# Kernel tuning notes

Hardware: AMD Instinct MI355X
Metric: run time of the kernel (lower is better)

The kernel has to match this reference:

```python
import jax, jax.numpy as jnp
import numpy as np

BS, QLEN, DIM, NH = 4, 2048, 1024, 16
DH = DIM // NH
NEG = float(np.finfo(np.float32).min)


def setup_inputs() -> dict:
    key = jax.random.key(0)
    ks = jax.random.split(key, 10)
    s = 1.0 / np.sqrt(DIM)
    return {
        "hidden_states": jax.random.normal(ks[0], (BS, QLEN, DIM), jnp.float32),
        "attention_mask": jnp.ones((BS, QLEN), jnp.int32),
        "Wq": jax.random.normal(ks[1], (DIM, DIM), jnp.float32) * s,
        "bq": jnp.zeros((DIM,), jnp.float32),
        "Wk": jax.random.normal(ks[2], (DIM, DIM), jnp.float32) * s,
        "bk": jnp.zeros((DIM,), jnp.float32),
        "Wv": jax.random.normal(ks[3], (DIM, DIM), jnp.float32) * s,
        "bv": jnp.zeros((DIM,), jnp.float32),
        "Wo": jax.random.normal(ks[4], (DIM, DIM), jnp.float32) * s,
        "bo": jnp.zeros((DIM,), jnp.float32),
    }


def _heads(x, bs):
    # [bs, len, dim] -> [bs, n_heads, len, dim_per_head]
    return x.reshape(bs, -1, NH, DH).transpose(0, 2, 1, 3)


def reference(hidden_states, attention_mask, Wq, bq, Wk, bk, Wv, bv, Wo, bo):
    bs, qlen, dim = hidden_states.shape
    q = _heads(hidden_states @ Wq.T + bq, bs) / jnp.sqrt(jnp.asarray(DH, hidden_states.dtype))
    k = _heads(hidden_states @ Wk.T + bk, bs)
    v = _heads(hidden_states @ Wv.T + bv, bs)
    scores = jnp.einsum("bhqd,bhkd->bhqk", q, k)  # [bs, nh, qlen, klen]
    mask = (attention_mask == 0)[:, None, None, :]  # [bs,1,1,klen]
    scores = jnp.where(mask, NEG, scores)
    weights = jax.nn.softmax(scores.astype(jnp.float32), axis=-1).astype(scores.dtype)
    context = jnp.einsum("bhqk,bhkd->bhqd", weights, v)
    context = context.transpose(0, 2, 1, 3).reshape(bs, qlen, dim)
    return context @ Wo.T + bo
```

## Files before the change

kernel.cpp:

```cpp
#include <hip/hip_runtime.h>
#include <hip/hip_bf16.h>

#define BS 4
#define QLEN 2048
#define DIM 1024
#define NH 16
#define DH 64

typedef __attribute__((ext_vector_type(8))) short bf16x8;
typedef __attribute__((ext_vector_type(4))) float f32x4;
typedef __attribute__((ext_vector_type(16))) float f32x16;
typedef __attribute__((ext_vector_type(2))) unsigned int u32x2;
typedef __attribute__((ext_vector_type(4))) unsigned int u32x4;
typedef unsigned short u16;
typedef unsigned int u32;
typedef unsigned long long u64;

#define LOG2E 1.44269504088896f

__device__ __forceinline__ u32 cvtpk_bf16(float lo, float hi) {
    u32 r;
    asm("v_cvt_pk_bf16_f32 %0, %1, %2" : "=v"(r) : "v"(lo), "v"(hi));
    return r;
}
__device__ __forceinline__ u16 f2bf_hw(float f) { return (u16)cvtpk_bf16(f, f); }

__device__ __forceinline__ void async_lds16(const void* gp, void* lp) {
    __builtin_amdgcn_global_load_lds(
        (const __attribute__((address_space(1))) u32*)(u64)gp,
        (__attribute__((address_space(3))) u32*)(u32)(u64)lp,
        16, 0, 0);
}

__global__ void cvt_fused(const float* __restrict__ H,
                          const float* __restrict__ W0, const float* __restrict__ W1,
                          const float* __restrict__ W2, const float* __restrict__ W3,
                          u16* __restrict__ Hb,
                          u16* __restrict__ D0, u16* __restrict__ D1,
                          u16* __restrict__ D2, u16* __restrict__ D3) {
    const int h4 = (BS * QLEN * DIM) / 4;
    int i = blockIdx.x * blockDim.x + threadIdx.x;
    const float* s;
    u16* d;
    int off;
    if (i < h4) { s = H; d = Hb; off = i; }
    else {
        int j = i - h4;
        int ws = j >> 18;
        off = j & 262143;
        s = ws == 0 ? W0 : ws == 1 ? W1 : ws == 2 ? W2 : W3;
        d = ws == 0 ? D0 : ws == 1 ? D1 : ws == 2 ? D2 : D3;
    }
    float4 v = ((const float4*)s)[off];
    uint2 o;
    o.x = cvtpk_bf16(v.x, v.y);
    o.y = cvtpk_bf16(v.z, v.w);
    ((uint2*)d)[off] = o;
}

__global__ void mask_prep(const int* __restrict__ mask, float* __restrict__ maskF,
                          int* __restrict__ flags) {
    const int tile = blockIdx.x;
    const int lane = threadIdx.x;
    const int idx = tile * 64 + lane;
    const int v = mask[idx];
    maskF[idx] = v ? 1.0f : 0.0f;
    u64 bal = __ballot(v == 0);
    if (lane == 0) flags[tile] = (bal != 0ull) ? 1 : 0;
}

__global__ __launch_bounds__(256) void gemm_qkv(
    const u16* __restrict__ Hb,
    const u16* __restrict__ Wq, const u16* __restrict__ Wk, const u16* __restrict__ Wv,
    const float* __restrict__ bq, const float* __restrict__ bk, const float* __restrict__ bvv,
    u16* __restrict__ Qb, u16* __restrict__ KF, u16* __restrict__ VF)
{
    __shared__ __align__(16) u16 As[2][128 * 32];
    __shared__ __align__(16) u16 Bs[2][128 * 32];
    const int z = blockIdx.z;
    const u16* W = z == 0 ? Wq : z == 1 ? Wk : Wv;
    const float* bias = z == 0 ? bq : z == 1 ? bk : bvv;
    const int t = threadIdx.x;
    const int w = t >> 6, lane = t & 63;
    const int lr = lane & 15, lg = lane >> 4;
    const int m0 = blockIdx.y * 128, n0 = blockIdx.x * 128;
    const int wm = (w >> 1) * 64, wn = (w & 1) * 64;
    const int srow = w * 16 + (lane >> 2);
    const int sk = (lane & 3) * 8;

    f32x4 acc[4][4] = {};

    auto STAGE = [&](int B, int kt) {
        async_lds16(Hb + (u64)(m0 + srow) * DIM + kt + sk,      &As[B][(w * 16) * 32]);
        async_lds16(Hb + (u64)(m0 + 64 + srow) * DIM + kt + sk, &As[B][(64 + w * 16) * 32]);
        async_lds16(W + (u64)(n0 + srow) * DIM + kt + sk,       &Bs[B][(w * 16) * 32]);
        async_lds16(W + (u64)(n0 + 64 + srow) * DIM + kt + sk,  &Bs[B][(64 + w * 16) * 32]);
    };

    STAGE(0, 0);
    int buf = 0;
    for (int kt = 0; kt < DIM; kt += 32) {
        asm volatile("s_waitcnt vmcnt(0)" ::: "memory");
        __builtin_amdgcn_s_barrier();
        __builtin_amdgcn_sched_barrier(0);
        if (kt + 32 < DIM) STAGE(buf ^ 1, kt + 32);
        bf16x8 a[4], b[4];
#pragma unroll
        for (int i = 0; i < 4; ++i) a[i] = *(const bf16x8*)&As[buf][(wm + i * 16 + lr) * 32 + lg * 8];
#pragma unroll
        for (int i = 0; i < 4; ++i) b[i] = *(const bf16x8*)&Bs[buf][(wn + i * 16 + lr) * 32 + lg * 8];
#pragma unroll
        for (int mi = 0; mi < 4; ++mi)
#pragma unroll
            for (int ni = 0; ni < 4; ++ni)
                acc[mi][ni] = __builtin_amdgcn_mfma_f32_16x16x32_bf16(a[mi], b[ni], acc[mi][ni], 0, 0, 0);
        buf ^= 1;
    }

#pragma unroll
    for (int mi = 0; mi < 4; ++mi)
#pragma unroll
        for (int ni = 0; ni < 4; ++ni) {
            const int col = n0 + wn + ni * 16 + lr;
            const float bb = bias[col];
#pragma unroll
            for (int r = 0; r < 4; ++r) {
                const int row = m0 + wm + mi * 16 + lg * 4 + r;
                const float v = acc[mi][ni][r] + bb;
                const int bh = (row >> 11) * NH + (col >> 6);
                const int q = row & (QLEN - 1);
                const int d = col & (DH - 1);
                if (z == 0) {
                    Qb[((u64)bh * QLEN + q) * DH + d] = f2bf_hw(v * (0.125f * LOG2E));
                } else if (z == 1) {
                    const int ktile = q >> 6, kb2 = (q >> 5) & 1, kl5 = q & 31;
                    const int c = d >> 3, dcc = c >> 1, chi = c & 1, j = d & 7;
                    KF[(u64)bh * QLEN * DH +
                       ((((u64)ktile * 2 + kb2) * 4 + dcc) * 64 + chi * 32 + kl5) * 8 + j] = f2bf_hw(v);
                } else {
                    const int ktile = q >> 6, kin = q & 63;
                    const int c = kin >> 3, kcc = c >> 1, chi = c & 1, j = kin & 7;
                    const int db = d >> 5, vl5 = d & 31;
                    VF[(u64)bh * QLEN * DH +
                       ((((u64)ktile * 2 + db) * 4 + kcc) * 64 + chi * 32 + vl5) * 8 + j] = f2bf_hw(v);
                }
            }
        }
}

__global__ __launch_bounds__(256) void gemm_o(
    const u16* __restrict__ A, const u16* __restrict__ W,
    const float* __restrict__ bias, float* __restrict__ ofp)
{
    __shared__ __align__(16) u16 As[2][128 * 32];
    __shared__ __align__(16) u16 Bs[2][128 * 32];
    const int t = threadIdx.x;
    const int w = t >> 6, lane = t & 63;
    const int lr = lane & 15, lg = lane >> 4;
    const int m0 = blockIdx.y * 128, n0 = blockIdx.x * 128;
    const int wm = (w >> 1) * 64, wn = (w & 1) * 64;
    const int srow = w * 16 + (lane >> 2);
    const int sk = (lane & 3) * 8;

    f32x4 acc[4][4] = {};

    auto STAGE = [&](int B, int kt) {
        async_lds16(A + (u64)(m0 + srow) * DIM + kt + sk,      &As[B][(w * 16) * 32]);
        async_lds16(A + (u64)(m0 + 64 + srow) * DIM + kt + sk, &As[B][(64 + w * 16) * 32]);
        async_lds16(W + (u64)(n0 + srow) * DIM + kt + sk,      &Bs[B][(w * 16) * 32]);
        async_lds16(W + (u64)(n0 + 64 + srow) * DIM + kt + sk, &Bs[B][(64 + w * 16) * 32]);
    };

    STAGE(0, 0);
    int buf = 0;
    for (int kt = 0; kt < DIM; kt += 32) {
        asm volatile("s_waitcnt vmcnt(0)" ::: "memory");
        __builtin_amdgcn_s_barrier();
        __builtin_amdgcn_sched_barrier(0);
        if (kt + 32 < DIM) STAGE(buf ^ 1, kt + 32);
        bf16x8 a[4], b[4];
#pragma unroll
        for (int i = 0; i < 4; ++i) a[i] = *(const bf16x8*)&As[buf][(wm + i * 16 + lr) * 32 + lg * 8];
#pragma unroll
        for (int i = 0; i < 4; ++i) b[i] = *(const bf16x8*)&Bs[buf][(wn + i * 16 + lr) * 32 + lg * 8];
#pragma unroll
        for (int mi = 0; mi < 4; ++mi)
#pragma unroll
            for (int ni = 0; ni < 4; ++ni)
                acc[mi][ni] = __builtin_amdgcn_mfma_f32_16x16x32_bf16(a[mi], b[ni], acc[mi][ni], 0, 0, 0);
        buf ^= 1;
    }

#pragma unroll
    for (int mi = 0; mi < 4; ++mi)
#pragma unroll
        for (int ni = 0; ni < 4; ++ni) {
            const int col = n0 + wn + ni * 16 + lr;
            const float bb = bias[col];
#pragma unroll
            for (int r = 0; r < 4; ++r) {
                const int row = m0 + wm + mi * 16 + lg * 4 + r;
                ofp[(u64)row * DIM + col] = acc[mi][ni][r] + bb;
            }
        }
}

struct KTile { bf16x8 f[2][4]; };

__global__ __launch_bounds__(256) void attn_kernel(
    const u16* __restrict__ Qb, const u16* __restrict__ KF, const u16* __restrict__ VF,
    const float* __restrict__ maskF, const int* __restrict__ mflags, u16* __restrict__ ctx)
{
    const int t = threadIdx.x;
    const int w = t >> 6, lane = t & 63;
    const int l5 = lane & 31, hi = lane >> 5;

    const int id = blockIdx.x + 16 * blockIdx.y;
    const int v = (id & 7) * 128 + (id >> 3);
    const int qt = v & 15, bh = v >> 4;
    const int b = bh >> 4, hh = bh & 15;
    const int q0 = qt * 128;

    const u16* kfl = KF + (u64)bh * QLEN * DH + (u64)lane * 8;
    const u16* vfl = VF + (u64)bh * QLEN * DH + (u64)lane * 8;
    const float* mFb = maskF + b * QLEN;
    const int* flb = mflags + b * (QLEN / 64);
    const u64 fmask = __ballot(flb[lane & 31] != 0);

    const u16* qp = Qb + ((u64)bh * QLEN + q0 + w * 32 + l5) * DH + hi * 8;
    bf16x8 bq[4];
#pragma unroll
    for (int dc = 0; dc < 4; ++dc) bq[dc] = *(const bf16x8*)(qp + dc * 16);

    f32x16 o[2] = {};
    float mrun = -3.0e38f, lsum = 0.f;

    auto loadK = [&](KTile& kk, int KT) {
        const u16* base = kfl + (u64)KT * 4096;
#pragma unroll
        for (int kb = 0; kb < 2; ++kb)
#pragma unroll
            for (int dc = 0; dc < 4; ++dc)
                kk.f[kb][dc] = *(const bf16x8*)(base + (kb * 4 + dc) * 512);
    };

    auto tile = [&](const KTile& kk, int kt64) {
        const u16* vb = vfl + (u64)kt64 * 4096;
        bf16x8 av0[4], av1[4];
#pragma unroll
        for (int kc = 0; kc < 4; ++kc) {
            av0[kc] = *(const bf16x8*)(vb + kc * 512);
            av1[kc] = *(const bf16x8*)(vb + (4 + kc) * 512);
        }

        f32x16 s0 = {}, s1 = {};
        __builtin_amdgcn_s_setprio(1);
#pragma unroll
        for (int dc = 0; dc < 4; ++dc) {
            s0 = __builtin_amdgcn_mfma_f32_32x32x16_bf16(kk.f[0][dc], bq[dc], s0, 0, 0, 0);
            s1 = __builtin_amdgcn_mfma_f32_32x32x16_bf16(kk.f[1][dc], bq[dc], s1, 0, 0, 0);
        }
        __builtin_amdgcn_s_setprio(0);

        float mx[16];
#pragma unroll
        for (int i = 0; i < 16; ++i) mx[i] = fmaxf(s0[i], s1[i]);
#pragma unroll
        for (int st = 8; st > 0; st >>= 1)
#pragma unroll
            for (int i = 0; i < 16; ++i) if (i < st) mx[i] = fmaxf(mx[i], mx[i + st]);
        const float tma = fmaxf(mx[0], __shfl_xor(mx[0], 32));

        if (!__all(tma <= mrun + 11.5415603f)) {
            const float nm = fmaxf(mrun, tma);
            const float corr = exp2f(mrun - nm);
            mrun = nm;
            lsum *= corr;
#pragma unroll
            for (int i = 0; i < 16; ++i) { o[0][i] *= corr; o[1][i] *= corr; }
        }

#pragma unroll
        for (int i = 0; i < 16; ++i) {
            s0[i] = exp2f(s0[i] - mrun);
            s1[i] = exp2f(s1[i] - mrun);
        }

        if ((fmask >> kt64) & 1ull) {
#pragma unroll
            for (int kb = 0; kb < 2; ++kb) {
                f32x16& sk = kb == 0 ? s0 : s1;
#pragma unroll
                for (int m = 0; m < 4; ++m) {
                    float4 mm = *(const float4*)&mFb[kt64 * 64 + kb * 32 + m * 8 + hi * 4];
                    sk[4 * m + 0] *= mm.x;
                    sk[4 * m + 1] *= mm.y;
                    sk[4 * m + 2] *= mm.z;
                    sk[4 * m + 3] *= mm.w;
                }
            }
        }

        {
            float ps[16];
#pragma unroll
            for (int i = 0; i < 16; ++i) ps[i] = s0[i] + s1[i];
#pragma unroll
            for (int st = 8; st > 0; st >>= 1)
#pragma unroll
                for (int i = 0; i < 16; ++i) if (i < st) ps[i] += ps[i + st];
            lsum += ps[0];
        }

        __builtin_amdgcn_s_setprio(1);
#pragma unroll
        for (int kc = 0; kc < 4; ++kc) {
            const f32x16& sk = (kc >> 1) == 0 ? s0 : s1;
            const int base = 8 * (kc & 1);
            const u32 P00 = cvtpk_bf16(sk[base + 0], sk[base + 1]);
            const u32 P01 = cvtpk_bf16(sk[base + 2], sk[base + 3]);
            const u32 P10 = cvtpk_bf16(sk[base + 4], sk[base + 5]);
            const u32 P11 = cvtpk_bf16(sk[base + 6], sk[base + 7]);
            u32x2 w02 = __builtin_amdgcn_permlane32_swap(P00, P10, false, false);
            u32x2 w13 = __builtin_amdgcn_permlane32_swap(P01, P11, false, false);
            u32x4 words;
            words.x = w02[0]; words.y = w13[0]; words.z = w02[1]; words.w = w13[1];
            const bf16x8 bp = __builtin_bit_cast(bf16x8, words);

            o[0] = __builtin_amdgcn_mfma_f32_32x32x16_bf16(av0[kc], bp, o[0], 0, 0, 0);
            o[1] = __builtin_amdgcn_mfma_f32_32x32x16_bf16(av1[kc], bp, o[1], 0, 0, 0);
        }
        __builtin_amdgcn_s_setprio(0);
    };

    KTile kA, kB;
    loadK(kA, 0);
    for (int tt = 0; tt < 32; tt += 2) {
        loadK(kB, tt + 1);
        tile(kA, tt);
        if (tt + 2 < 32) loadK(kA, tt + 2);
        tile(kB, tt + 1);
    }

    const float lall = lsum + __shfl_xor(lsum, 32);
    const float inv = 1.0f / fmaxf(lall, 1e-37f);

    u16* cp = ctx + (((u64)b * QLEN + (q0 + w * 32 + l5)) * NH + hh) * DH;
#pragma unroll
    for (int db = 0; db < 2; ++db)
#pragma unroll
        for (int m = 0; m < 4; ++m) {
            const int d0 = db * 32 + m * 8 + hi * 4;
            const u32 wA = cvtpk_bf16(o[db][4 * m + 0] * inv, o[db][4 * m + 1] * inv);
            const u32 wB = cvtpk_bf16(o[db][4 * m + 2] * inv, o[db][4 * m + 3] * inv);
            *(u32*)(cp + d0) = wA;
            *(u32*)(cp + d0 + 2) = wB;
        }
}

extern "C" void kernel_launch(void* const* d_in, const int* in_sizes, int n_in,
                              void* d_out, int out_size, void* d_ws, size_t ws_size,
                              hipStream_t stream) {
    const float* H    = (const float*)d_in[0];
    const int*   mask = (const int*)d_in[1];
    const float* Wq   = (const float*)d_in[2];
    const float* bq   = (const float*)d_in[3];
    const float* Wk   = (const float*)d_in[4];
    const float* bk   = (const float*)d_in[5];
    const float* Wv   = (const float*)d_in[6];
    const float* bv   = (const float*)d_in[7];
    const float* Wo   = (const float*)d_in[8];
    const float* bo   = (const float*)d_in[9];
    float* out = (float*)d_out;

    const u64 NTOK = (u64)BS * QLEN;
    const u64 HN = NTOK * DIM;
    const u64 WN = (u64)DIM * DIM;

    u16* Hb  = (u16*)d_ws;
    u16* Wqb = Hb + HN;
    u16* Wkb = Wqb + WN;
    u16* Wvb = Wkb + WN;
    u16* Wob = Wvb + WN;
    u16* Qb  = Wob + WN;
    u16* KFb = Qb + HN;
    u16* VFb = KFb + HN;
    u16* Ctx = VFb + HN;
    float* maskF = (float*)(Ctx + HN);
    int* mflags = (int*)(maskF + BS * QLEN);

    cvt_fused<<<12288, 256, 0, stream>>>(H, Wq, Wk, Wv, Wo, Hb, Wqb, Wkb, Wvb, Wob);
    mask_prep<<<BS * (QLEN / 64), 64, 0, stream>>>(mask, maskF, mflags);

    gemm_qkv<<<dim3(DIM / 128, (int)(NTOK / 128), 3), 256, 0, stream>>>(
        Hb, Wqb, Wkb, Wvb, bq, bk, bv, Qb, KFb, VFb);

    attn_kernel<<<dim3(QLEN / 128, BS * NH), 256, 0, stream>>>(Qb, KFb, VFb, maskF, mflags, Ctx);

    gemm_o<<<dim3(DIM / 128, (int)(NTOK / 128)), 256, 0, stream>>>(Ctx, Wob, bo, out);
}
```

Baseline: 239.4 us.

## Software-pipeline QK of next tile with softmax and PV of current tile

Splits the per-tile attention body into QK, softmax and PV stages and interleaves them so the next tile's QK MFMAs are issued while the current tile's softmax runs. This aims to overlap matrix-core work with the VALU exp/max/sum work. V loads are moved from the start of each tile into the PV loop right before use, which shortens their register lifetime but exposes their latency. Two extra score accumulators raise register pressure and could cut occupancy.

Result: slower. 254.9 us (+6.5%).

```diff
diff --git a/kernel.cpp b/kernel.cpp
--- a/kernel.cpp
+++ b/kernel.cpp
@@ -244,16 +244,9 @@
                 kk.f[kb][dc] = *(const bf16x8*)(base + (kb * 4 + dc) * 512);
     };
 
-    auto tile = [&](const KTile& kk, int kt64) {
-        const u16* vb = vfl + (u64)kt64 * 4096;
-        bf16x8 av0[4], av1[4];
-#pragma unroll
-        for (int kc = 0; kc < 4; ++kc) {
-            av0[kc] = *(const bf16x8*)(vb + kc * 512);
-            av1[kc] = *(const bf16x8*)(vb + (4 + kc) * 512);
-        }
-
-        f32x16 s0 = {}, s1 = {};
+    auto QK = [&](f32x16& s0, f32x16& s1, const KTile& kk) {
+        s0 = f32x16{};
+        s1 = f32x16{};
         __builtin_amdgcn_s_setprio(1);
 #pragma unroll
         for (int dc = 0; dc < 4; ++dc) {
@@ -261,7 +254,9 @@
             s1 = __builtin_amdgcn_mfma_f32_32x32x16_bf16(kk.f[1][dc], bq[dc], s1, 0, 0, 0);
         }
         __builtin_amdgcn_s_setprio(0);
-
+    };
+
+    auto SM = [&](f32x16& s0, f32x16& s1, int kt64) {
         float mx[16];
 #pragma unroll
         for (int i = 0; i < 16; ++i) mx[i] = fmaxf(s0[i], s1[i]);
@@ -301,17 +296,18 @@
             }
         }
 
-        {
-            float ps[16];
-#pragma unroll
-            for (int i = 0; i < 16; ++i) ps[i] = s0[i] + s1[i];
-#pragma unroll
-            for (int st = 8; st > 0; st >>= 1)
-#pragma unroll
-                for (int i = 0; i < 16; ++i) if (i < st) ps[i] += ps[i + st];
-            lsum += ps[0];
-        }
-
+        float ps[16];
+#pragma unroll
+        for (int i = 0; i < 16; ++i) ps[i] = s0[i] + s1[i];
+#pragma unroll
+        for (int st = 8; st > 0; st >>= 1)
+#pragma unroll
+            for (int i = 0; i < 16; ++i) if (i < st) ps[i] += ps[i + st];
+        lsum += ps[0];
+    };
+
+    auto PV = [&](const f32x16& s0, const f32x16& s1, int kt64) {
+        const u16* vb = vfl + (u64)kt64 * 4096;
         __builtin_amdgcn_s_setprio(1);
 #pragma unroll
         for (int kc = 0; kc < 4; ++kc) {
@@ -327,20 +323,37 @@
             words.x = w02[0]; words.y = w13[0]; words.z = w02[1]; words.w = w13[1];
             const bf16x8 bp = __builtin_bit_cast(bf16x8, words);
 
-            o[0] = __builtin_amdgcn_mfma_f32_32x32x16_bf16(av0[kc], bp, o[0], 0, 0, 0);
-            o[1] = __builtin_amdgcn_mfma_f32_32x32x16_bf16(av1[kc], bp, o[1], 0, 0, 0);
+            bf16x8 av0 = *(const bf16x8*)(vb + kc * 512);
+            bf16x8 av1 = *(const bf16x8*)(vb + (4 + kc) * 512);
+            o[0] = __builtin_amdgcn_mfma_f32_32x32x16_bf16(av0, bp, o[0], 0, 0, 0);
+            o[1] = __builtin_amdgcn_mfma_f32_32x32x16_bf16(av1, bp, o[1], 0, 0, 0);
         }
         __builtin_amdgcn_s_setprio(0);
     };
 
+    f32x16 sX0, sX1, sY0, sY1;
     KTile kA, kB;
+
     loadK(kA, 0);
-    for (int tt = 0; tt < 32; tt += 2) {
-        loadK(kB, tt + 1);
-        tile(kA, tt);
-        if (tt + 2 < 32) loadK(kA, tt + 2);
-        tile(kB, tt + 1);
+    loadK(kB, 1);
+    QK(sX0, sX1, kA);
+
+    for (int tt = 0; tt < 30; tt += 2) {
+        SM(sX0, sX1, tt);
+        QK(sY0, sY1, kB);
+        loadK(kA, tt + 2);
+        PV(sX0, sX1, tt);
+
+        SM(sY0, sY1, tt + 1);
+        QK(sX0, sX1, kA);
+        if (tt + 3 < 32) loadK(kB, tt + 3);
+        PV(sY0, sY1, tt + 1);
     }
+    SM(sX0, sX1, 30);
+    QK(sY0, sY1, kB);
+    PV(sX0, sX1, 30);
+    SM(sY0, sY1, 31);
+    PV(sY0, sY1, 31);
 
     const float lall = lsum + __shfl_xor(lsum, 32);
     const float inv = 1.0f / fmaxf(lall, 1e-37f);
```
